# Kernel optimization log

Measured on AMD Instinct MI355X. Metric: run time of the kernel, lower is better.

## Reference

```python
import jax, jax.numpy as jnp
import numpy as np

N, HIDDEN, HEADS = 4096, 256, 8
HEAD = HIDDEN // HEADS


def setup_inputs() -> dict:
    key = jax.random.key(0)
    ks = jax.random.split(key, 10)
    s = 1.0 / np.sqrt(HIDDEN)
    return {
        "x": jax.random.normal(ks[0], (N, HIDDEN), jnp.float32),
        "Adj": jax.random.randint(ks[1], (N, N), 0, 2, jnp.int32),
        "wq_w": jax.random.normal(ks[2], (HIDDEN, HIDDEN), jnp.float32) * s,
        "wq_b": jax.random.normal(ks[3], (HIDDEN,), jnp.float32) * s,
        "wk_w": jax.random.normal(ks[4], (HIDDEN, HIDDEN), jnp.float32) * s,
        "wk_b": jax.random.normal(ks[5], (HIDDEN,), jnp.float32) * s,
        "wv_w": jax.random.normal(ks[6], (HIDDEN, HIDDEN), jnp.float32) * s,
        "wv_b": jax.random.normal(ks[7], (HIDDEN,), jnp.float32) * s,
        "wo_w": jax.random.normal(ks[8], (HIDDEN, HIDDEN), jnp.float32) * s,
        "wo_b": jax.random.normal(ks[9], (HIDDEN,), jnp.float32) * s,
    }


def reference(x, Adj, wq_w, wq_b, wk_w, wk_b, wv_w, wv_b, wo_w, wo_b):
    n = x.shape[0]
    # torch nn.Linear: y = x @ W.T + b
    q = (x @ wq_w.T + wq_b).reshape(n, HEADS, HEAD).transpose(1, 0, 2)  # [H,N,Dh]
    # k is computed in the original but unused due to a bug (q @ v^T below)
    k = (x @ wk_w.T + wk_b).reshape(n, HEADS, HEAD).transpose(1, 0, 2)  # noqa: F841
    v = (x @ wv_w.T + wv_b).reshape(n, HEADS, HEAD).transpose(1, 0, 2)  # [H,N,Dh]
    # Faithful to original bug: attention scores use v, not k
    scores = jnp.einsum("hnd,hmd->hnm", q, v) / np.sqrt(HEAD).astype(np.float32)
    scores = jnp.where(Adj[None, :, :] == 0, jnp.float32(-1e9), scores)
    attn = jax.nn.softmax(scores, axis=-1)  # [H,N,N]
    out = jnp.einsum("hnm,hmd->hnd", attn, v)  # [H,N,Dh]
    out = out.transpose(1, 0, 2).reshape(n, HIDDEN)
    return out @ wo_w.T + wo_b, attn
```

## Files before the change

kernel.cpp:

```cpp
#include <hip/hip_runtime.h>
#include <hip/hip_bf16.h>
#include <stdint.h>

#define NN   4096
#define HIDN 256
#define NHD  8
#define HD   32

typedef __attribute__((ext_vector_type(8))) short short8;
typedef __attribute__((ext_vector_type(4))) float f32x4;

static __device__ __forceinline__ unsigned short f2bf(float f) {
  __hip_bfloat16 h = __float2bfloat16(f);
  return __builtin_bit_cast(unsigned short, h);
}
static __device__ __forceinline__ float bf2f(unsigned short u) {
  __hip_bfloat16 h = __builtin_bit_cast(__hip_bfloat16, u);
  return __bfloat162float(h);
}

__global__ __launch_bounds__(256) void mhg_qv_kernel(
    const float* __restrict__ x,
    const float* __restrict__ wq_w, const float* __restrict__ wq_b,
    const float* __restrict__ wv_w, const float* __restrict__ wv_b,
    unsigned short* __restrict__ Qhi, unsigned short* __restrict__ Qlo,
    unsigned short* __restrict__ Vhi, unsigned short* __restrict__ Vlo,
    unsigned short* __restrict__ Vt)
{
  const int o  = threadIdx.x;
  const int r0 = blockIdx.x * 8;
  float aq[8], av[8];
#pragma unroll
  for (int r = 0; r < 8; ++r) { aq[r] = 0.f; av[r] = 0.f; }
  const float4* wq4 = (const float4*)(wq_w + (size_t)o * HIDN);
  const float4* wv4 = (const float4*)(wv_w + (size_t)o * HIDN);
  const float* xb = x + (size_t)r0 * HIDN;
  for (int k0 = 0; k0 < HIDN / 4; ++k0) {
    float4 wq = wq4[k0];
    float4 wv = wv4[k0];
#pragma unroll
    for (int r = 0; r < 8; ++r) {
      float4 xv = *(const float4*)(xb + r * HIDN + k0 * 4);
      aq[r] = fmaf(xv.x, wq.x, fmaf(xv.y, wq.y, fmaf(xv.z, wq.z, fmaf(xv.w, wq.w, aq[r]))));
      av[r] = fmaf(xv.x, wv.x, fmaf(xv.y, wv.y, fmaf(xv.z, wv.z, fmaf(xv.w, wv.w, av[r]))));
    }
  }
  const float bq = wq_b[o], bv = wv_b[o];
  constexpr float CS = (float)(1.4426950408889634 / 5.656854249492380195206754896838);
  alignas(16) unsigned short vt8[8];
#pragma unroll
  for (int r = 0; r < 8; ++r) {
    float qv = (aq[r] + bq) * CS;
    unsigned short qh = f2bf(qv);
    unsigned short ql = f2bf(qv - bf2f(qh));
    float vv = av[r] + bv;
    unsigned short vh = f2bf(vv);
    unsigned short vl = f2bf(vv - bf2f(vh));
    size_t idx = (size_t)(r0 + r) * HIDN + o;
    Qhi[idx] = qh; Qlo[idx] = ql;
    Vhi[idx] = vh; Vlo[idx] = vl;
    vt8[r] = vh;
  }
  *(uint4*)(Vt + (size_t)o * NN + r0) = *(const uint4*)vt8;
}

__global__ __launch_bounds__(64) void mhg_attn_kernel(
    const int* __restrict__ Adj,
    const unsigned short* __restrict__ Qhi, const unsigned short* __restrict__ Qlo,
    const unsigned short* __restrict__ Vhi, const unsigned short* __restrict__ Vlo,
    const unsigned short* __restrict__ Vt,
    float* __restrict__ attn, float* __restrict__ O)
{
  const int lane = threadIdx.x & 63;
  const int n    = lane & 15;
  const int qd   = lane >> 4;
  const int h    = blockIdx.x & (NHD - 1);
  const int rb   = blockIdx.x >> 3;
  const int wr0  = rb * 16;

  __shared__ uint64_t maskB[256][4];
  __shared__ __align__(16) unsigned short Plds[16][40];

  const size_t hoff = (size_t)h * HD + qd * 8;
  const short8 a_hi = *(const short8*)(Qhi + (size_t)(wr0 + n) * HIDN + hoff);
  const short8 a_lo = *(const short8*)(Qlo + (size_t)(wr0 + n) * HIDN + hoff);
  const unsigned short* pVh = Vhi + (size_t)n * HIDN + hoff;
  const unsigned short* pVl = Vlo + (size_t)n * HIDN + hoff;
  const size_t adjb = (size_t)(wr0 + 4 * qd) * NN + n;

  float l0 = 0.f, l1 = 0.f, l2 = 0.f, l3 = 0.f;

  short8 bh = *(const short8*)(pVh);
  short8 bl = *(const short8*)(pVl);
  int a0 = Adj[adjb], a1 = Adj[adjb + NN], a2 = Adj[adjb + 2 * NN], a3 = Adj[adjb + 3 * NN];

  for (int c = 0; c < 256; ++c) {
    const int cn = (c < 255) ? c + 1 : 255;
    short8 bhn = *(const short8*)(pVh + (size_t)cn * (16 * HIDN));
    short8 bln = *(const short8*)(pVl + (size_t)cn * (16 * HIDN));
    const size_t ab = adjb + (size_t)cn * 16;
    int a0n = Adj[ab], a1n = Adj[ab + NN], a2n = Adj[ab + 2 * NN], a3n = Adj[ab + 3 * NN];

    f32x4 acc = {0.f, 0.f, 0.f, 0.f};
    acc = __builtin_amdgcn_mfma_f32_16x16x32_bf16(a_hi, bh, acc, 0, 0, 0);
    acc = __builtin_amdgcn_mfma_f32_16x16x32_bf16(a_lo, bh, acc, 0, 0, 0);
    acc = __builtin_amdgcn_mfma_f32_16x16x32_bf16(a_hi, bl, acc, 0, 0, 0);

    uint64_t m0 = __ballot(a0 != 0);
    uint64_t m1 = __ballot(a1 != 0);
    uint64_t m2 = __ballot(a2 != 0);
    uint64_t m3 = __ballot(a3 != 0);
    if (lane == 0) { maskB[c][0] = m0; maskB[c][1] = m1; maskB[c][2] = m2; maskB[c][3] = m3; }

    l0 += a0 ? __builtin_amdgcn_exp2f(acc[0]) : 0.f;
    l1 += a1 ? __builtin_amdgcn_exp2f(acc[1]) : 0.f;
    l2 += a2 ? __builtin_amdgcn_exp2f(acc[2]) : 0.f;
    l3 += a3 ? __builtin_amdgcn_exp2f(acc[3]) : 0.f;

    bh = bhn; bl = bln; a0 = a0n; a1 = a1n; a2 = a2n; a3 = a3n;
  }

  float r0v, r1v, r2v, r3v;
  {
    float s;
    s = l0; s += __shfl_xor(s, 1, 16); s += __shfl_xor(s, 2, 16); s += __shfl_xor(s, 4, 16); s += __shfl_xor(s, 8, 16); r0v = 1.0f / s;
    s = l1; s += __shfl_xor(s, 1, 16); s += __shfl_xor(s, 2, 16); s += __shfl_xor(s, 4, 16); s += __shfl_xor(s, 8, 16); r1v = 1.0f / s;
    s = l2; s += __shfl_xor(s, 1, 16); s += __shfl_xor(s, 2, 16); s += __shfl_xor(s, 4, 16); s += __shfl_xor(s, 8, 16); r2v = 1.0f / s;
    s = l3; s += __shfl_xor(s, 1, 16); s += __shfl_xor(s, 2, 16); s += __shfl_xor(s, 4, 16); s += __shfl_xor(s, 8, 16); r3v = 1.0f / s;
  }

  f32x4 oc0 = {0.f, 0.f, 0.f, 0.f}, oc1 = {0.f, 0.f, 0.f, 0.f};
  const unsigned short* pVt0 = Vt + (size_t)(h * HD + n) * NN + qd * 8;
  const unsigned short* pVt1 = pVt0 + (size_t)16 * NN;
  float* pAt = attn + (size_t)h * NN * NN + (size_t)(wr0 + 4 * qd) * NN + n;

  short8 bh0 = *(const short8*)(pVh);
  short8 bl0 = *(const short8*)(pVl);
  short8 bh1 = *(const short8*)(pVh + 16 * HIDN);
  short8 bl1 = *(const short8*)(pVl + 16 * HIDN);
  short8 vb0 = *(const short8*)(pVt0);
  short8 vb1 = *(const short8*)(pVt1);

  for (int cp = 0; cp < 128; ++cp) {
    const int np = (cp < 127) ? cp + 1 : 127;
    short8 bh0n = *(const short8*)(pVh + (size_t)(2 * np) * (16 * HIDN));
    short8 bl0n = *(const short8*)(pVl + (size_t)(2 * np) * (16 * HIDN));
    short8 bh1n = *(const short8*)(pVh + (size_t)(2 * np + 1) * (16 * HIDN));
    short8 bl1n = *(const short8*)(pVl + (size_t)(2 * np + 1) * (16 * HIDN));
    short8 vb0n = *(const short8*)(pVt0 + (size_t)np * 32);
    short8 vb1n = *(const short8*)(pVt1 + (size_t)np * 32);

    {
      const int c = 2 * cp;
      const size_t c0 = (size_t)c * 16;
      f32x4 acc = {0.f, 0.f, 0.f, 0.f};
      acc = __builtin_amdgcn_mfma_f32_16x16x32_bf16(a_hi, bh0, acc, 0, 0, 0);
      acc = __builtin_amdgcn_mfma_f32_16x16x32_bf16(a_lo, bh0, acc, 0, 0, 0);
      acc = __builtin_amdgcn_mfma_f32_16x16x32_bf16(a_hi, bl0, acc, 0, 0, 0);
      uint64_t m0 = maskB[c][0], m1 = maskB[c][1], m2 = maskB[c][2], m3 = maskB[c][3];
      float p0 = ((m0 >> lane) & 1) ? __builtin_amdgcn_exp2f(acc[0]) * r0v : 0.f;
      float p1 = ((m1 >> lane) & 1) ? __builtin_amdgcn_exp2f(acc[1]) * r1v : 0.f;
      float p2 = ((m2 >> lane) & 1) ? __builtin_amdgcn_exp2f(acc[2]) * r2v : 0.f;
      float p3 = ((m3 >> lane) & 1) ? __builtin_amdgcn_exp2f(acc[3]) * r3v : 0.f;
      pAt[c0] = p0; pAt[c0 + NN] = p1; pAt[c0 + 2 * NN] = p2; pAt[c0 + 3 * NN] = p3;
      Plds[4 * qd + 0][n] = f2bf(p0);
      Plds[4 * qd + 1][n] = f2bf(p1);
      Plds[4 * qd + 2][n] = f2bf(p2);
      Plds[4 * qd + 3][n] = f2bf(p3);
    }
    {
      const int c = 2 * cp + 1;
      const size_t c0 = (size_t)c * 16;
      f32x4 acc = {0.f, 0.f, 0.f, 0.f};
      acc = __builtin_amdgcn_mfma_f32_16x16x32_bf16(a_hi, bh1, acc, 0, 0, 0);
      acc = __builtin_amdgcn_mfma_f32_16x16x32_bf16(a_lo, bh1, acc, 0, 0, 0);
      acc = __builtin_amdgcn_mfma_f32_16x16x32_bf16(a_hi, bl1, acc, 0, 0, 0);
      uint64_t m0 = maskB[c][0], m1 = maskB[c][1], m2 = maskB[c][2], m3 = maskB[c][3];
      float p0 = ((m0 >> lane) & 1) ? __builtin_amdgcn_exp2f(acc[0]) * r0v : 0.f;
      float p1 = ((m1 >> lane) & 1) ? __builtin_amdgcn_exp2f(acc[1]) * r1v : 0.f;
      float p2 = ((m2 >> lane) & 1) ? __builtin_amdgcn_exp2f(acc[2]) * r2v : 0.f;
      float p3 = ((m3 >> lane) & 1) ? __builtin_amdgcn_exp2f(acc[3]) * r3v : 0.f;
      pAt[c0] = p0; pAt[c0 + NN] = p1; pAt[c0 + 2 * NN] = p2; pAt[c0 + 3 * NN] = p3;
      Plds[4 * qd + 0][16 + n] = f2bf(p0);
      Plds[4 * qd + 1][16 + n] = f2bf(p1);
      Plds[4 * qd + 2][16 + n] = f2bf(p2);
      Plds[4 * qd + 3][16 + n] = f2bf(p3);
    }
    __asm__ volatile("" ::: "memory");
    __builtin_amdgcn_s_waitcnt(0xC07F);
    __asm__ volatile("" ::: "memory");
    short8 ap = *(const short8*)&Plds[n][qd * 8];
    oc0 = __builtin_amdgcn_mfma_f32_16x16x32_bf16(ap, vb0, oc0, 0, 0, 0);
    oc1 = __builtin_amdgcn_mfma_f32_16x16x32_bf16(ap, vb1, oc1, 0, 0, 0);

    bh0 = bh0n; bl0 = bl0n; bh1 = bh1n; bl1 = bl1n; vb0 = vb0n; vb1 = vb1n;
  }

  const int orow = wr0 + 4 * qd;
#pragma unroll
  for (int r = 0; r < 4; ++r) {
    O[(size_t)(orow + r) * HIDN + h * HD + n]      = oc0[r];
    O[(size_t)(orow + r) * HIDN + h * HD + 16 + n] = oc1[r];
  }
}

__global__ __launch_bounds__(256) void mhg_oproj_kernel(
    const float* __restrict__ O,
    const float* __restrict__ wo_w, const float* __restrict__ wo_b,
    float* __restrict__ out)
{
  const int o  = threadIdx.x;
  const int r0 = blockIdx.x * 8;
  float ac[8];
#pragma unroll
  for (int r = 0; r < 8; ++r) ac[r] = 0.f;
  const float4* wo4 = (const float4*)(wo_w + (size_t)o * HIDN);
  const float* Ob = O + (size_t)r0 * HIDN;
  for (int k0 = 0; k0 < HIDN / 4; ++k0) {
    float4 w = wo4[k0];
#pragma unroll
    for (int r = 0; r < 8; ++r) {
      float4 xv = *(const float4*)(Ob + r * HIDN + k0 * 4);
      ac[r] = fmaf(xv.x, w.x, fmaf(xv.y, w.y, fmaf(xv.z, w.z, fmaf(xv.w, w.w, ac[r]))));
    }
  }
  const float b = wo_b[o];
#pragma unroll
  for (int r = 0; r < 8; ++r)
    out[(size_t)(r0 + r) * HIDN + o] = ac[r] + b;
}

extern "C" void kernel_launch(void* const* d_in, const int* in_sizes, int n_in,
                              void* d_out, int out_size, void* d_ws, size_t ws_size,
                              hipStream_t stream) {
  (void)in_sizes; (void)n_in; (void)out_size; (void)ws_size;
  const float* x    = (const float*)d_in[0];
  const int*   Adj  = (const int*)d_in[1];
  const float* wq_w = (const float*)d_in[2];
  const float* wq_b = (const float*)d_in[3];
  const float* wv_w = (const float*)d_in[6];
  const float* wv_b = (const float*)d_in[7];
  const float* wo_w = (const float*)d_in[8];
  const float* wo_b = (const float*)d_in[9];

  float* out  = (float*)d_out;
  float* attn = out + (size_t)NN * HIDN;

  unsigned short* Qhi = (unsigned short*)d_ws;
  unsigned short* Qlo = Qhi + (size_t)NN * HIDN;
  unsigned short* Vhi = Qlo + (size_t)NN * HIDN;
  unsigned short* Vlo = Vhi + (size_t)NN * HIDN;
  unsigned short* Vt  = Vlo + (size_t)NN * HIDN;
  float*          Oacc = (float*)(Vt + (size_t)NN * HIDN);

  hipLaunchKernelGGL(mhg_qv_kernel, dim3(NN / 8), dim3(256), 0, stream,
                     x, wq_w, wq_b, wv_w, wv_b, Qhi, Qlo, Vhi, Vlo, Vt);
  hipLaunchKernelGGL(mhg_attn_kernel, dim3(NHD * (NN / 16)), dim3(64), 0, stream,
                     Adj, Qhi, Qlo, Vhi, Vlo, Vt, attn, Oacc);
  hipLaunchKernelGGL(mhg_oproj_kernel, dim3(NN / 8), dim3(256), 0, stream,
                     Oacc, wo_w, wo_b, out);
}
```

Before: 930.5 us.

## Split attention key range across four waves per block with LDS reductions

The attention kernel grows from one wave to four waves per 16-row block. Each wave handles a quarter of the key columns in both passes, and the row sums and partial outputs are combined through shared memory with two block barriers. Each lane now keeps its adjacency bits in per-lane 64-bit masks instead of a ballot table in LDS, and the attention-matrix writes become nontemporal stores. The goal is more parallelism per output tile and lower latency per block, at the cost of extra LDS traffic, barriers and higher register pressure under launch bounds of 256 threads with 8 blocks.

```diff
diff --git a/kernel.cpp b/kernel.cpp
--- a/kernel.cpp
+++ b/kernel.cpp
@@ -64,22 +64,25 @@
   *(uint4*)(Vt + (size_t)o * NN + r0) = *(const uint4*)vt8;
 }
 
-__global__ __launch_bounds__(64) void mhg_attn_kernel(
+__global__ __launch_bounds__(256, 8) void mhg_attn_kernel(
     const int* __restrict__ Adj,
     const unsigned short* __restrict__ Qhi, const unsigned short* __restrict__ Qlo,
     const unsigned short* __restrict__ Vhi, const unsigned short* __restrict__ Vlo,
     const unsigned short* __restrict__ Vt,
     float* __restrict__ attn, float* __restrict__ O)
 {
-  const int lane = threadIdx.x & 63;
+  const int tid  = threadIdx.x;
+  const int lane = tid & 63;
+  const int wv   = tid >> 6;
   const int n    = lane & 15;
   const int qd   = lane >> 4;
   const int h    = blockIdx.x & (NHD - 1);
   const int rb   = blockIdx.x >> 3;
   const int wr0  = rb * 16;
 
-  __shared__ uint64_t maskB[256][4];
-  __shared__ __align__(16) unsigned short Plds[16][40];
+  __shared__ __align__(16) unsigned short Plds[4][16][40];
+  __shared__ float Lpart[4][16];
+  __shared__ float Opart[4][16][33];
 
   const size_t hoff = (size_t)h * HD + qd * 8;
   const short8 a_hi = *(const short8*)(Qhi + (size_t)(wr0 + n) * HIDN + hoff);
@@ -88,14 +91,20 @@
   const unsigned short* pVl = Vlo + (size_t)n * HIDN + hoff;
   const size_t adjb = (size_t)(wr0 + 4 * qd) * NN + n;
 
+  const int c0w = wv * 64;
+
   float l0 = 0.f, l1 = 0.f, l2 = 0.f, l3 = 0.f;
-
-  short8 bh = *(const short8*)(pVh);
-  short8 bl = *(const short8*)(pVl);
-  int a0 = Adj[adjb], a1 = Adj[adjb + NN], a2 = Adj[adjb + 2 * NN], a3 = Adj[adjb + 3 * NN];
-
-  for (int c = 0; c < 256; ++c) {
-    const int cn = (c < 255) ? c + 1 : 255;
+  uint64_t m0 = 0, m1 = 0, m2 = 0, m3 = 0;
+
+  short8 bh = *(const short8*)(pVh + (size_t)c0w * (16 * HIDN));
+  short8 bl = *(const short8*)(pVl + (size_t)c0w * (16 * HIDN));
+  {
+  }
+  size_t ab0 = adjb + (size_t)c0w * 16;
+  int a0 = Adj[ab0], a1 = Adj[ab0 + NN], a2 = Adj[ab0 + 2 * NN], a3 = Adj[ab0 + 3 * NN];
+
+  for (int cc = 0; cc < 64; ++cc) {
+    const int cn = c0w + ((cc < 63) ? cc + 1 : 63);
     short8 bhn = *(const short8*)(pVh + (size_t)cn * (16 * HIDN));
     short8 bln = *(const short8*)(pVl + (size_t)cn * (16 * HIDN));
     const size_t ab = adjb + (size_t)cn * 16;
@@ -106,11 +115,10 @@
     acc = __builtin_amdgcn_mfma_f32_16x16x32_bf16(a_lo, bh, acc, 0, 0, 0);
     acc = __builtin_amdgcn_mfma_f32_16x16x32_bf16(a_hi, bl, acc, 0, 0, 0);
 
-    uint64_t m0 = __ballot(a0 != 0);
-    uint64_t m1 = __ballot(a1 != 0);
-    uint64_t m2 = __ballot(a2 != 0);
-    uint64_t m3 = __ballot(a3 != 0);
-    if (lane == 0) { maskB[c][0] = m0; maskB[c][1] = m1; maskB[c][2] = m2; maskB[c][3] = m3; }
+    m0 |= (uint64_t)(a0 != 0) << cc;
+    m1 |= (uint64_t)(a1 != 0) << cc;
+    m2 |= (uint64_t)(a2 != 0) << cc;
+    m3 |= (uint64_t)(a3 != 0) << cc;
 
     l0 += a0 ? __builtin_amdgcn_exp2f(acc[0]) : 0.f;
     l1 += a1 ? __builtin_amdgcn_exp2f(acc[1]) : 0.f;
@@ -120,29 +128,41 @@
     bh = bhn; bl = bln; a0 = a0n; a1 = a1n; a2 = a2n; a3 = a3n;
   }
 
-  float r0v, r1v, r2v, r3v;
   {
     float s;
-    s = l0; s += __shfl_xor(s, 1, 16); s += __shfl_xor(s, 2, 16); s += __shfl_xor(s, 4, 16); s += __shfl_xor(s, 8, 16); r0v = 1.0f / s;
-    s = l1; s += __shfl_xor(s, 1, 16); s += __shfl_xor(s, 2, 16); s += __shfl_xor(s, 4, 16); s += __shfl_xor(s, 8, 16); r1v = 1.0f / s;
-    s = l2; s += __shfl_xor(s, 1, 16); s += __shfl_xor(s, 2, 16); s += __shfl_xor(s, 4, 16); s += __shfl_xor(s, 8, 16); r2v = 1.0f / s;
-    s = l3; s += __shfl_xor(s, 1, 16); s += __shfl_xor(s, 2, 16); s += __shfl_xor(s, 4, 16); s += __shfl_xor(s, 8, 16); r3v = 1.0f / s;
-  }
+    s = l0; s += __shfl_xor(s, 1, 16); s += __shfl_xor(s, 2, 16); s += __shfl_xor(s, 4, 16); s += __shfl_xor(s, 8, 16); l0 = s;
+    s = l1; s += __shfl_xor(s, 1, 16); s += __shfl_xor(s, 2, 16); s += __shfl_xor(s, 4, 16); s += __shfl_xor(s, 8, 16); l1 = s;
+    s = l2; s += __shfl_xor(s, 1, 16); s += __shfl_xor(s, 2, 16); s += __shfl_xor(s, 4, 16); s += __shfl_xor(s, 8, 16); l2 = s;
+    s = l3; s += __shfl_xor(s, 1, 16); s += __shfl_xor(s, 2, 16); s += __shfl_xor(s, 4, 16); s += __shfl_xor(s, 8, 16); l3 = s;
+  }
+  if (n == 0) {
+    Lpart[wv][4 * qd + 0] = l0;
+    Lpart[wv][4 * qd + 1] = l1;
+    Lpart[wv][4 * qd + 2] = l2;
+    Lpart[wv][4 * qd + 3] = l3;
+  }
+  __syncthreads();
+  const float r0v = 1.0f / (Lpart[0][4 * qd + 0] + Lpart[1][4 * qd + 0] + Lpart[2][4 * qd + 0] + Lpart[3][4 * qd + 0]);
+  const float r1v = 1.0f / (Lpart[0][4 * qd + 1] + Lpart[1][4 * qd + 1] + Lpart[2][4 * qd + 1] + Lpart[3][4 * qd + 1]);
+  const float r2v = 1.0f / (Lpart[0][4 * qd + 2] + Lpart[1][4 * qd + 2] + Lpart[2][4 * qd + 2] + Lpart[3][4 * qd + 2]);
+  const float r3v = 1.0f / (Lpart[0][4 * qd + 3] + Lpart[1][4 * qd + 3] + Lpart[2][4 * qd + 3] + Lpart[3][4 * qd + 3]);
 
   f32x4 oc0 = {0.f, 0.f, 0.f, 0.f}, oc1 = {0.f, 0.f, 0.f, 0.f};
   const unsigned short* pVt0 = Vt + (size_t)(h * HD + n) * NN + qd * 8;
   const unsigned short* pVt1 = pVt0 + (size_t)16 * NN;
   float* pAt = attn + (size_t)h * NN * NN + (size_t)(wr0 + 4 * qd) * NN + n;
 
-  short8 bh0 = *(const short8*)(pVh);
-  short8 bl0 = *(const short8*)(pVl);
-  short8 bh1 = *(const short8*)(pVh + 16 * HIDN);
-  short8 bl1 = *(const short8*)(pVl + 16 * HIDN);
-  short8 vb0 = *(const short8*)(pVt0);
-  short8 vb1 = *(const short8*)(pVt1);
-
-  for (int cp = 0; cp < 128; ++cp) {
-    const int np = (cp < 127) ? cp + 1 : 127;
+  const int cp0 = wv * 32;
+  short8 bh0 = *(const short8*)(pVh + (size_t)(2 * cp0) * (16 * HIDN));
+  short8 bl0 = *(const short8*)(pVl + (size_t)(2 * cp0) * (16 * HIDN));
+  short8 bh1 = *(const short8*)(pVh + (size_t)(2 * cp0 + 1) * (16 * HIDN));
+  short8 bl1 = *(const short8*)(pVl + (size_t)(2 * cp0 + 1) * (16 * HIDN));
+  short8 vb0 = *(const short8*)(pVt0 + (size_t)cp0 * 32);
+  short8 vb1 = *(const short8*)(pVt1 + (size_t)cp0 * 32);
+
+  for (int i = 0; i < 32; ++i) {
+    const int cp = cp0 + i;
+    const int np = cp0 + ((i < 31) ? i + 1 : 31);
     short8 bh0n = *(const short8*)(pVh + (size_t)(2 * np) * (16 * HIDN));
     short8 bl0n = *(const short8*)(pVl + (size_t)(2 * np) * (16 * HIDN));
     short8 bh1n = *(const short8*)(pVh + (size_t)(2 * np + 1) * (16 * HIDN));
@@ -152,55 +172,70 @@
 
     {
       const int c = 2 * cp;
+      const int cl = 2 * i;
       const size_t c0 = (size_t)c * 16;
       f32x4 acc = {0.f, 0.f, 0.f, 0.f};
       acc = __builtin_amdgcn_mfma_f32_16x16x32_bf16(a_hi, bh0, acc, 0, 0, 0);
       acc = __builtin_amdgcn_mfma_f32_16x16x32_bf16(a_lo, bh0, acc, 0, 0, 0);
       acc = __builtin_amdgcn_mfma_f32_16x16x32_bf16(a_hi, bl0, acc, 0, 0, 0);
-      uint64_t m0 = maskB[c][0], m1 = maskB[c][1], m2 = maskB[c][2], m3 = maskB[c][3];
-      float p0 = ((m0 >> lane) & 1) ? __builtin_amdgcn_exp2f(acc[0]) * r0v : 0.f;
-      float p1 = ((m1 >> lane) & 1) ? __builtin_amdgcn_exp2f(acc[1]) * r1v : 0.f;
-      float p2 = ((m2 >> lane) & 1) ? __builtin_amdgcn_exp2f(acc[2]) * r2v : 0.f;
-      float p3 = ((m3 >> lane) & 1) ? __builtin_amdgcn_exp2f(acc[3]) * r3v : 0.f;
-      pAt[c0] = p0; pAt[c0 + NN] = p1; pAt[c0 + 2 * NN] = p2; pAt[c0 + 3 * NN] = p3;
-      Plds[4 * qd + 0][n] = f2bf(p0);
-      Plds[4 * qd + 1][n] = f2bf(p1);
-      Plds[4 * qd + 2][n] = f2bf(p2);
-      Plds[4 * qd + 3][n] = f2bf(p3);
+      float p0 = ((m0 >> cl) & 1) ? __builtin_amdgcn_exp2f(acc[0]) * r0v : 0.f;
+      float p1 = ((m1 >> cl) & 1) ? __builtin_amdgcn_exp2f(acc[1]) * r1v : 0.f;
+      float p2 = ((m2 >> cl) & 1) ? __builtin_amdgcn_exp2f(acc[2]) * r2v : 0.f;
+      float p3 = ((m3 >> cl) & 1) ? __builtin_amdgcn_exp2f(acc[3]) * r3v : 0.f;
+      __builtin_nontemporal_store(p0, &pAt[c0]);
+      __builtin_nontemporal_store(p1, &pAt[c0 + NN]);
+      __builtin_nontemporal_store(p2, &pAt[c0 + 2 * NN]);
+      __builtin_nontemporal_store(p3, &pAt[c0 + 3 * NN]);
+      Plds[wv][4 * qd + 0][n] = f2bf(p0);
+      Plds[wv][4 * qd + 1][n] = f2bf(p1);
+      Plds[wv][4 * qd + 2][n] = f2bf(p2);
+      Plds[wv][4 * qd + 3][n] = f2bf(p3);
     }
     {
       const int c = 2 * cp + 1;
+      const int cl = 2 * i + 1;
       const size_t c0 = (size_t)c * 16;
       f32x4 acc = {0.f, 0.f, 0.f, 0.f};
       acc = __builtin_amdgcn_mfma_f32_16x16x32_bf16(a_hi, bh1, acc, 0, 0, 0);
       acc = __builtin_amdgcn_mfma_f32_16x16x32_bf16(a_lo, bh1, acc, 0, 0, 0);
       acc = __builtin_amdgcn_mfma_f32_16x16x32_bf16(a_hi, bl1, acc, 0, 0, 0);
-      uint64_t m0 = maskB[c][0], m1 = maskB[c][1], m2 = maskB[c][2], m3 = maskB[c][3];
-      float p0 = ((m0 >> lane) & 1) ? __builtin_amdgcn_exp2f(acc[0]) * r0v : 0.f;
-      float p1 = ((m1 >> lane) & 1) ? __builtin_amdgcn_exp2f(acc[1]) * r1v : 0.f;
-      float p2 = ((m2 >> lane) & 1) ? __builtin_amdgcn_exp2f(acc[2]) * r2v : 0.f;
-      float p3 = ((m3 >> lane) & 1) ? __builtin_amdgcn_exp2f(acc[3]) * r3v : 0.f;
-      pAt[c0] = p0; pAt[c0 + NN] = p1; pAt[c0 + 2 * NN] = p2; pAt[c0 + 3 * NN] = p3;
-      Plds[4 * qd + 0][16 + n] = f2bf(p0);
-      Plds[4 * qd + 1][16 + n] = f2bf(p1);
-      Plds[4 * qd + 2][16 + n] = f2bf(p2);
-      Plds[4 * qd + 3][16 + n] = f2bf(p3);
+      float p0 = ((m0 >> cl) & 1) ? __builtin_amdgcn_exp2f(acc[0]) * r0v : 0.f;
+      float p1 = ((m1 >> cl) & 1) ? __builtin_amdgcn_exp2f(acc[1]) * r1v : 0.f;
+      float p2 = ((m2 >> cl) & 1) ? __builtin_amdgcn_exp2f(acc[2]) * r2v : 0.f;
+      float p3 = ((m3 >> cl) & 1) ? __builtin_amdgcn_exp2f(acc[3]) * r3v : 0.f;
+      __builtin_nontemporal_store(p0, &pAt[c0]);
+      __builtin_nontemporal_store(p1, &pAt[c0 + NN]);
+      __builtin_nontemporal_store(p2, &pAt[c0 + 2 * NN]);
+      __builtin_nontemporal_store(p3, &pAt[c0 + 3 * NN]);
+      Plds[wv][4 * qd + 0][16 + n] = f2bf(p0);
+      Plds[wv][4 * qd + 1][16 + n] = f2bf(p1);
+      Plds[wv][4 * qd + 2][16 + n] = f2bf(p2);
+      Plds[wv][4 * qd + 3][16 + n] = f2bf(p3);
     }
     __asm__ volatile("" ::: "memory");
     __builtin_amdgcn_s_waitcnt(0xC07F);
     __asm__ volatile("" ::: "memory");
-    short8 ap = *(const short8*)&Plds[n][qd * 8];
+    short8 ap = *(const short8*)&Plds[wv][n][qd * 8];
     oc0 = __builtin_amdgcn_mfma_f32_16x16x32_bf16(ap, vb0, oc0, 0, 0, 0);
     oc1 = __builtin_amdgcn_mfma_f32_16x16x32_bf16(ap, vb1, oc1, 0, 0, 0);
 
     bh0 = bh0n; bl0 = bl0n; bh1 = bh1n; bl1 = bl1n; vb0 = vb0n; vb1 = vb1n;
   }
 
-  const int orow = wr0 + 4 * qd;
 #pragma unroll
   for (int r = 0; r < 4; ++r) {
-    O[(size_t)(orow + r) * HIDN + h * HD + n]      = oc0[r];
-    O[(size_t)(orow + r) * HIDN + h * HD + 16 + n] = oc1[r];
+    Opart[wv][4 * qd + r][n]      = oc0[r];
+    Opart[wv][4 * qd + r][16 + n] = oc1[r];
+  }
+  __syncthreads();
+  {
+    const int e   = tid * 2;
+    const int row = e >> 5;
+    const int col = e & 31;
+    float s0 = Opart[0][row][col]     + Opart[1][row][col]     + Opart[2][row][col]     + Opart[3][row][col];
+    float s1 = Opart[0][row][col + 1] + Opart[1][row][col + 1] + Opart[2][row][col + 1] + Opart[3][row][col + 1];
+    O[(size_t)(wr0 + row) * HIDN + h * HD + col]     = s0;
+    O[(size_t)(wr0 + row) * HIDN + h * HD + col + 1] = s1;
   }
 }
 
@@ -255,7 +290,7 @@
 
   hipLaunchKernelGGL(mhg_qv_kernel, dim3(NN / 8), dim3(256), 0, stream,
                      x, wq_w, wq_b, wv_w, wv_b, Qhi, Qlo, Vhi, Vlo, Vt);
-  hipLaunchKernelGGL(mhg_attn_kernel, dim3(NHD * (NN / 16)), dim3(64), 0, stream,
+  hipLaunchKernelGGL(mhg_attn_kernel, dim3(NHD * (NN / 16)), dim3(256), 0, stream,
                      Adj, Qhi, Qlo, Vhi, Vlo, Vt, attn, Oacc);
   hipLaunchKernelGGL(mhg_oproj_kernel, dim3(NN / 8), dim3(256), 0, stream,
                      Oacc, wo_w, wo_b, out);
```

Result: slower. 1.057 ms (+13.6%).
